# Kernel tuning notes

Measured on AMD Instinct MI355X. Metric: run time of the kernel, lower is better.

## Reference

```python
import jax, jax.numpy as jnp
import numpy as np

B, S, E, DK, DV = 8, 2048, 1024, 512, 512
MASK = True


def setup_inputs() -> dict:
    key = jax.random.key(0)
    ks = jax.random.split(key, 12)
    def xavier(k, shape):
        fan_in, fan_out = shape[1], shape[0]
        lim = float(np.sqrt(6.0 / (fan_in + fan_out)))
        return jax.random.uniform(k, shape, jnp.float32, -lim, lim)
    return {
        "x": jax.random.normal(ks[0], (B, S, E), jnp.float32),
        "Wq_w": xavier(ks[1], (DK, E)),
        "Wq_b": jax.random.normal(ks[2], (DK,), jnp.float32) * 0.02,
        "Wk_w": xavier(ks[3], (DK, E)),
        "Wk_b": jax.random.normal(ks[4], (DK,), jnp.float32) * 0.02,
        "Wv_w": xavier(ks[5], (DV, E)),
        "Wv_b": jax.random.normal(ks[6], (DV,), jnp.float32) * 0.02,
        "alphaq": jax.random.normal(ks[7], (S,), jnp.float32) * 0.1,
        "alphav": jax.random.normal(ks[8], (S,), jnp.float32) * 0.1,
        "tokenq": xavier(ks[9], (DK, DK)),
        "tokenv": xavier(ks[10], (DV, DV)),
    }


def reference(x, Wq_w, Wq_b, Wk_w, Wk_b, Wv_w, Wv_b, alphaq, alphav, tokenq, tokenv):
    dk = Wk_w.shape[0]
    seq_len = x.shape[1]
    Q = jnp.einsum("bse,ke->bsk", x, Wq_w) + Wq_b
    K = jnp.einsum("bse,ke->bsk", x, Wk_w) + Wk_b
    V = jnp.einsum("bse,ve->bsv", x, Wv_w) + Wv_b

    # token-aware temperatures: tanh(tokenX @ gelu(X)^T)^T == tanh(gelu(X) @ tokenX^T)
    token_temp_q = jnp.tanh(jnp.einsum("bsj,ij->bsi", jax.nn.gelu(Q, approximate=False), tokenq))
    token_temp_v = jnp.tanh(jnp.einsum("bsj,ij->bsi", jax.nn.gelu(V, approximate=False), tokenv))

    # argmax/gather knobs: [B,S,S] scores -> K_max per query
    attn_map_exps = jnp.einsum("bqk,bsk->bqs", Q, K)
    max_ids = jnp.argmax(attn_map_exps, axis=2)                    # [B,S]
    K_max = jnp.take_along_axis(K, max_ids[:, :, None], axis=1)    # [B,S,DK]
    K_sum = jnp.sum(K, axis=1, keepdims=True)                      # [B,1,DK]
    knobs = jnp.abs(Q * (K_sum - seq_len * K_max))                 # [B,S,DK]

    log_pos = jnp.log(jnp.arange(1, seq_len + 1, dtype=jnp.float32))[None, :, None]  # [1,S,1]
    position_temp_q = 1.0 + jax.nn.sigmoid(alphaq[None, :, None] - knobs) * log_pos
    position_temp_v = 1.0 + jax.nn.sigmoid(alphav)[None, :, None] * log_pos

    gated_Q = (position_temp_q + token_temp_q) * Q
    gated_V = (position_temp_v + token_temp_v) * V

    attention_wts = jnp.einsum("bqk,bsk->bqs", gated_Q, K) / jnp.sqrt(jnp.float32(dk))
    if MASK:
        causal = jnp.triu(jnp.ones((seq_len, seq_len), dtype=bool), k=1)
        attention_wts = jnp.where(causal[None], -jnp.inf, attention_wts)
    attention_scores = jax.nn.softmax(attention_wts.astype(jnp.float32), axis=-1)
    return jnp.einsum("bqs,bsv->bqv", attention_scores, gated_V)
```

## Files before the change

kernel.cpp:

```cpp
#include <hip/hip_runtime.h>
#include <hip/hip_bf16.h>
#include <math.h>

typedef unsigned short u16;
typedef __attribute__((ext_vector_type(8))) short bhalf8;
typedef __attribute__((ext_vector_type(4))) float floatx4;

#define MFMA16(a,b,c) __builtin_amdgcn_mfma_f32_16x16x32_bf16((a),(b),(c),0,0,0)

__device__ __forceinline__ float bf2f(u16 u){ return __uint_as_float(((unsigned)u)<<16); }
__device__ __forceinline__ u16 f2bf(float f){
  unsigned u = __float_as_uint(f);
  u += 0x7fffu + ((u>>16)&1u);
  return (u16)(u>>16);
}
__device__ __forceinline__ float gelu_f(float x){ return 0.5f*x*(1.0f+erff(x*0.70710678118654752f)); }
__device__ __forceinline__ float sigm(float x){ return 1.0f/(1.0f+__expf(-x)); }

__global__ __launch_bounds__(256) void init_counts(int* cnt){
  if (threadIdx.x == 0 && blockIdx.x == 0) *cnt = 0;
}

__global__ __launch_bounds__(256) void cvt_f32_bf16(const float* __restrict__ src,
                                                    u16* __restrict__ dst, int n){
  int i = (blockIdx.x*256 + threadIdx.x)*4;
  if (i >= n) return;
  const float4 v = *(const float4*)(src + i);
  ushort4 o;
  o.x = f2bf(v.x); o.y = f2bf(v.y); o.z = f2bf(v.z); o.w = f2bf(v.w);
  *(ushort4*)(dst + i) = o;
}

__global__ __launch_bounds__(256) void cvt_split(const float* __restrict__ src,
                                                 u16* __restrict__ dsth,
                                                 u16* __restrict__ dstl, int n){
  int i = (blockIdx.x*256 + threadIdx.x)*4;
  if (i >= n) return;
  const float4 v = *(const float4*)(src + i);
  float vv[4] = {v.x, v.y, v.z, v.w};
  ushort4 oh, ol;
  u16 h;
  h = f2bf(vv[0]); oh.x = h; ol.x = f2bf(vv[0] - bf2f(h));
  h = f2bf(vv[1]); oh.y = h; ol.y = f2bf(vv[1] - bf2f(h));
  h = f2bf(vv[2]); oh.z = h; ol.z = f2bf(vv[2] - bf2f(h));
  h = f2bf(vv[3]); oh.w = h; ol.w = f2bf(vv[3] - bf2f(h));
  *(ushort4*)(dsth + i) = oh;
  *(ushort4*)(dstl + i) = ol;
}

template<int SPLIT>
__global__ __launch_bounds__(256) void gemm_qkvT(
    const u16* __restrict__ xh, const u16* __restrict__ xl,
    const u16* __restrict__ Whh, const u16* __restrict__ Whl,
    const float* __restrict__ bq, const float* __restrict__ bk, const float* __restrict__ bv,
    float* __restrict__ Qf, float* __restrict__ Kf, u16* __restrict__ Vb)
{
  __shared__ __align__(16) u16 Ah[128][72];
  __shared__ __align__(16) u16 Bh[128][72];
  __shared__ __align__(16) u16 Al[SPLIT?128:1][72];
  __shared__ __align__(16) u16 Bl[SPLIT?128:1][72];
  const int tid = threadIdx.x;
  const int lane = tid & 63, wid = tid >> 6;
  const int l15 = lane & 15, lg = lane >> 4;
  const int wr = wid >> 1, wc = wid & 1;
  const int m0 = blockIdx.y * 128;
  const int n0 = blockIdx.x * 128 + (SPLIT ? 0 : 1024);
  const int which = n0 >> 9;
  const int nb = n0 & 511;
  const float* bias = (which==0) ? bq : (which==1) ? bk : bv;

  floatx4 acc[4][4] = {};

  bhalf8 RAh[4], RBh[4], RAl[4], RBl[4];
  auto loadT = [&](int k0){
    #pragma unroll
    for (int it = 0; it < 4; ++it){
      int e = (tid + it*256)*8;
      int r = e >> 6, c = e & 63;
      size_t ao = (size_t)(m0+r)*1024 + k0 + c;
      size_t bo = (size_t)(n0+r)*1024 + k0 + c;
      RAh[it] = *(const bhalf8*)(xh + ao);
      RBh[it] = *(const bhalf8*)(Whh + bo);
      if (SPLIT){
        RAl[it] = *(const bhalf8*)(xl + ao);
        RBl[it] = *(const bhalf8*)(Whl + bo);
      }
    }
  };
  auto writeT = [&](){
    #pragma unroll
    for (int it = 0; it < 4; ++it){
      int e = (tid + it*256)*8;
      int r = e >> 6, c = e & 63;
      *(bhalf8*)&Ah[r][c] = RAh[it];
      *(bhalf8*)&Bh[r][c] = RBh[it];
      if (SPLIT){
        *(bhalf8*)&Al[r][c] = RAl[it];
        *(bhalf8*)&Bl[r][c] = RBl[it];
      }
    }
  };

  loadT(0);
  writeT();
  __syncthreads();
  for (int k0 = 0; k0 < 1024; k0 += 64){
    if (k0 < 960) loadT(k0 + 64);
    #pragma unroll
    for (int kk = 0; kk < 2; ++kk){
      bhalf8 ah[4], bh8[4];
      #pragma unroll
      for (int xx=0; xx<4; xx++){
        ah[xx]  = *(const bhalf8*)&Ah[wr*64 + xx*16 + l15][kk*32 + lg*8];
        bh8[xx] = *(const bhalf8*)&Bh[wc*64 + xx*16 + l15][kk*32 + lg*8];
      }
      if (SPLIT){
        bhalf8 al[4], bl8[4];
        #pragma unroll
        for (int xx=0; xx<4; xx++){
          al[xx]  = *(const bhalf8*)&Al[wr*64 + xx*16 + l15][kk*32 + lg*8];
          bl8[xx] = *(const bhalf8*)&Bl[wc*64 + xx*16 + l15][kk*32 + lg*8];
        }
        #pragma unroll
        for (int mi=0;mi<4;mi++)
          #pragma unroll
          for (int ni=0;ni<4;ni++){
            acc[mi][ni] = MFMA16(ah[mi], bh8[ni], acc[mi][ni]);
            acc[mi][ni] = MFMA16(ah[mi], bl8[ni], acc[mi][ni]);
            acc[mi][ni] = MFMA16(al[mi], bh8[ni], acc[mi][ni]);
          }
      } else {
        #pragma unroll
        for (int mi=0;mi<4;mi++)
          #pragma unroll
          for (int ni=0;ni<4;ni++)
            acc[mi][ni] = MFMA16(ah[mi], bh8[ni], acc[mi][ni]);
      }
    }
    __syncthreads();
    if (k0 < 960){
      writeT();
      __syncthreads();
    }
  }

  #pragma unroll
  for (int mi=0;mi<4;mi++)
    #pragma unroll
    for (int ni=0;ni<4;ni++){
      int cc = nb + wc*64 + ni*16 + l15;
      float bias_v = bias[cc];
      #pragma unroll
      for (int i=0;i<4;i++){
        int row = m0 + wr*64 + mi*16 + lg*4 + i;
        float v = acc[mi][ni][i] + bias_v;
        size_t off = (size_t)row*512 + cc;
        if (which==0){ Qf[off] = v; }
        else if (which==1){ Kf[off] = v; }
        else { Vb[off] = f2bf(v); }
      }
    }
}

__global__ __launch_bounds__(256) void gemm_tanh2(
    const float* __restrict__ Af, const u16* __restrict__ Ab,
    const u16* __restrict__ Bq, const u16* __restrict__ Bv,
    u16* __restrict__ oq, u16* __restrict__ ov)
{
  __shared__ __align__(16) u16 As[128][72];
  __shared__ __align__(16) u16 Bs[128][72];
  const int tid = threadIdx.x;
  const int lane = tid & 63, wid = tid >> 6;
  const int l15 = lane & 15, lg = lane >> 4;
  const int wr = wid >> 1, wc = wid & 1;
  const int m0 = blockIdx.y * 128, n0 = blockIdx.x * 128;
  const int zp = blockIdx.z;
  const u16* B = zp ? Bv : Bq;
  u16* o0 = zp ? ov : oq;

  floatx4 acc[4][4] = {};

  float4 RAf[8]; bhalf8 RAb[4]; bhalf8 RB[4];
  auto loadT = [&](int k0){
    #pragma unroll
    for (int it=0; it<4; ++it){
      int e = (tid + it*256)*8;
      int r = e >> 6, c = e & 63;
      if (zp == 0){
        const float* src = Af + (size_t)(m0+r)*512 + k0 + c;
        RAf[it*2]   = *(const float4*)src;
        RAf[it*2+1] = *(const float4*)(src+4);
      } else {
        RAb[it] = *(const bhalf8*)(Ab + (size_t)(m0+r)*512 + k0 + c);
      }
      RB[it] = *(const bhalf8*)(B + (size_t)(n0+r)*512 + k0 + c);
    }
  };
  auto writeT = [&](){
    #pragma unroll
    for (int it=0; it<4; ++it){
      int e = (tid + it*256)*8;
      int r = e >> 6, c = e & 63;
      bhalf8 g;
      if (zp == 0){
        float vv[8] = {RAf[it*2].x,RAf[it*2].y,RAf[it*2].z,RAf[it*2].w,
                       RAf[it*2+1].x,RAf[it*2+1].y,RAf[it*2+1].z,RAf[it*2+1].w};
        #pragma unroll
        for (int j=0;j<8;j++) g[j] = (short)f2bf(gelu_f(vv[j]));
      } else {
        #pragma unroll
        for (int j=0;j<8;j++) g[j] = (short)f2bf(gelu_f(bf2f((u16)RAb[it][j])));
      }
      *(bhalf8*)&As[r][c] = g;
      *(bhalf8*)&Bs[r][c] = RB[it];
    }
  };

  loadT(0);
  writeT();
  __syncthreads();
  for (int k0 = 0; k0 < 512; k0 += 64){
    if (k0 < 448) loadT(k0 + 64);
    #pragma unroll
    for (int kk = 0; kk < 2; ++kk){
      bhalf8 af[4], bfr[4];
      #pragma unroll
      for (int xx=0;xx<4;xx++) af[xx]  = *(const bhalf8*)&As[wr*64 + xx*16 + l15][kk*32 + lg*8];
      #pragma unroll
      for (int xx=0;xx<4;xx++) bfr[xx] = *(const bhalf8*)&Bs[wc*64 + xx*16 + l15][kk*32 + lg*8];
      #pragma unroll
      for (int mi=0;mi<4;mi++)
        #pragma unroll
        for (int ni=0;ni<4;ni++)
          acc[mi][ni] = MFMA16(af[mi], bfr[ni], acc[mi][ni]);
    }
    __syncthreads();
    if (k0 < 448){
      writeT();
      __syncthreads();
    }
  }

  #pragma unroll
  for (int mi=0;mi<4;mi++)
    #pragma unroll
    for (int ni=0;ni<4;ni++){
      int coln = n0 + wc*64 + ni*16 + l15;
      #pragma unroll
      for (int i=0;i<4;i++){
        int row = m0 + wr*64 + mi*16 + lg*4 + i;
        o0[(size_t)row*512 + coln] = f2bf(tanhf(acc[mi][ni][i]));
      }
    }
}

__global__ __launch_bounds__(256) void gemm_argmax(
    const u16* __restrict__ Qsh, const u16* __restrict__ Qsl,
    const u16* __restrict__ Ksh, const u16* __restrict__ Ksl,
    float4* __restrict__ part)
{
  __shared__ __align__(16) u16 Ah[128][40];
  __shared__ __align__(16) u16 Al[128][40];
  __shared__ __align__(16) u16 Bh[128][40];
  __shared__ __align__(16) u16 Bl[128][40];
  const int tid = threadIdx.x;
  const int lane = tid & 63, wid = tid >> 6;
  const int l15 = lane & 15, lg = lane >> 4;
  const int wr = wid >> 1, wc = wid & 1;
  const int lin = blockIdx.x + 16*blockIdx.y + 256*blockIdx.z;
  const int swz = (lin & 7)*256 + (lin >> 3);
  const int zb  = swz >> 8;
  const int rem = swz & 255;
  const int m0 = (rem >> 4) * 128;
  const int n0 = (rem & 15) * 128;
  const size_t bo = (size_t)zb * 2048 * 512;

  floatx4 acc[4][4] = {};

  bhalf8 RQh[2], RQl[2], RKh[2], RKl[2];
  auto loadT = [&](int k0){
    #pragma unroll
    for (int it = 0; it < 2; ++it){
      int e = (tid + it*256)*8;
      int r = e >> 5, c = e & 31;
      size_t qo = bo + (size_t)(m0+r)*512 + k0 + c;
      size_t ko = bo + (size_t)(n0+r)*512 + k0 + c;
      RQh[it] = *(const bhalf8*)(Qsh + qo);
      RQl[it] = *(const bhalf8*)(Qsl + qo);
      RKh[it] = *(const bhalf8*)(Ksh + ko);
      RKl[it] = *(const bhalf8*)(Ksl + ko);
    }
  };
  auto writeT = [&](){
    #pragma unroll
    for (int it = 0; it < 2; ++it){
      int e = (tid + it*256)*8;
      int r = e >> 5, c = e & 31;
      *(bhalf8*)&Ah[r][c] = RQh[it];
      *(bhalf8*)&Al[r][c] = RQl[it];
      *(bhalf8*)&Bh[r][c] = RKh[it];
      *(bhalf8*)&Bl[r][c] = RKl[it];
    }
  };

  loadT(0);
  writeT();
  __syncthreads();
  for (int k0 = 0; k0 < 512; k0 += 32){
    if (k0 < 480) loadT(k0 + 32);
    {
      bhalf8 ah[4], al[4], bh[4], bl[4];
      #pragma unroll
      for (int xx=0;xx<4;xx++){
        ah[xx] = *(const bhalf8*)&Ah[wr*64 + xx*16 + l15][lg*8];
        al[xx] = *(const bhalf8*)&Al[wr*64 + xx*16 + l15][lg*8];
        bh[xx] = *(const bhalf8*)&Bh[wc*64 + xx*16 + l15][lg*8];
        bl[xx] = *(const bhalf8*)&Bl[wc*64 + xx*16 + l15][lg*8];
      }
      #pragma unroll
      for (int mi=0;mi<4;mi++)
        #pragma unroll
        for (int ni=0;ni<4;ni++){
          acc[mi][ni] = MFMA16(ah[mi], bh[ni], acc[mi][ni]);
          acc[mi][ni] = MFMA16(ah[mi], bl[ni], acc[mi][ni]);
          acc[mi][ni] = MFMA16(al[mi], bh[ni], acc[mi][ni]);
        }
    }
    __syncthreads();
    if (k0 < 480){
      writeT();
      __syncthreads();
    }
  }

  #pragma unroll
  for (int mi=0;mi<4;mi++)
    #pragma unroll
    for (int i=0;i<4;i++){
      float v1 = -INFINITY, v2 = -INFINITY; int i1 = 0x7fffffff;
      #pragma unroll
      for (int ni=0;ni<4;ni++){
        float v = acc[mi][ni][i];
        int col = n0 + wc*64 + ni*16 + l15;
        if (v > v1 || (v == v1 && col < i1)){ v2 = v1; v1 = v; i1 = col; }
        else v2 = fmaxf(v2, v);
      }
      #pragma unroll
      for (int ms=1; ms<16; ms<<=1){
        float w1 = __shfl_xor(v1, ms, 64);
        int   j1 = __shfl_xor(i1, ms, 64);
        float w2 = __shfl_xor(v2, ms, 64);
        if (w1 > v1 || (w1 == v1 && j1 < i1)){ v2 = fmaxf(v1, w2); v1 = w1; i1 = j1; }
        else { v2 = fmaxf(v2, w1); }
      }
      if (l15 == 0){
        int row = m0 + wr*64 + mi*16 + lg*4 + i;
        size_t gm = (size_t)zb*2048 + row;
        part[gm*32 + ((n0>>7)<<1) + wc] = make_float4(v1, __int_as_float(i1), v2, 0.0f);
      }
    }
}

__global__ __launch_bounds__(256) void argmax_reduce(const float4* __restrict__ part,
                                                     int* __restrict__ ids,
                                                     int* __restrict__ list1,
                                                     int* __restrict__ cnt){
  int r = blockIdx.x*256 + threadIdx.x;
  if (r >= 16384) return;
  float v1 = -INFINITY, v2 = -INFINITY; int i1 = 0x7fffffff;
  #pragma unroll
  for (int t=0;t<32;t++){
    float4 p = part[(size_t)r*32 + t];
    float w1 = p.x, w2 = p.z; int j1 = __float_as_int(p.y);
    if (w1 > v1 || (w1 == v1 && j1 < i1)){ v2 = fmaxf(v1, w2); v1 = w1; i1 = j1; }
    else { v2 = fmaxf(v2, w1); }
  }
  ids[r] = i1;
  if (v1 - v2 < 0.02f){
    int k = atomicAdd(cnt, 1);
    if (k < 16384) list1[k] = r;
  }
}

__global__ __launch_bounds__(256) void argmax_fix(
    const float* __restrict__ Qf, const float* __restrict__ Kf,
    const int* __restrict__ list1, const int* __restrict__ cnt,
    int* __restrict__ ids)
{
  __shared__ float q[512];
  __shared__ double rbest[256];
  __shared__ int ridx[256];
  const int tid = threadIdx.x;
  const int n = *cnt;
  for (int j = blockIdx.x; j < n; j += gridDim.x){
    const int r = list1[j];
    const int b = r >> 11;
    __syncthreads();
    for (int d = tid; d < 512; d += 256) q[d] = Qf[(size_t)r*512 + d];
    __syncthreads();
    double best = -1e300; int bi = 0x7fffffff;
    for (int c = 0; c < 8; ++c){
      int key = tid + c*256;
      const float* kr = Kf + ((size_t)b*2048 + key)*512;
      double acc = 0.0;
      for (int e = 0; e < 512; ++e) acc += (double)q[e]*(double)kr[e];
      if (acc > best || (acc == best && key < bi)){ best = acc; bi = key; }
    }
    rbest[tid] = best; ridx[tid] = bi;
    __syncthreads();
    for (int st=128; st>0; st>>=1){
      if (tid < st){
        double ov = rbest[tid+st]; int oi = ridx[tid+st];
        if (ov > rbest[tid] || (ov == rbest[tid] && oi < ridx[tid])){ rbest[tid]=ov; ridx[tid]=oi; }
      }
      __syncthreads();
    }
    if (tid == 0) ids[r] = ridx[0];
    __syncthreads();
  }
}

__global__ __launch_bounds__(256) void ksum_part(const float* __restrict__ Kf,
                                                 float* __restrict__ kpart){
  const int b = blockIdx.x, chunk = blockIdx.y;
  const int tid = threadIdx.x;
  const float* base = Kf + (size_t)b*2048*512 + (size_t)chunk*128*512;
  #pragma unroll
  for (int h = 0; h < 2; ++h){
    int col = tid + h*256;
    double s = 0.0;
    for (int r = 0; r < 128; ++r) s += (double)base[(size_t)r*512 + col];
    kpart[((size_t)b*16 + chunk)*512 + col] = (float)s;
  }
}
__global__ __launch_bounds__(256) void ksum_final(const float* __restrict__ kpart,
                                                  float* __restrict__ Ksum){
  const int b = blockIdx.x >> 1;
  const int col = (blockIdx.x & 1)*256 + threadIdx.x;
  double s = 0.0;
  #pragma unroll
  for (int c = 0; c < 16; ++c) s += (double)kpart[((size_t)b*16 + c)*512 + col];
  Ksum[b*512 + col] = (float)s;
}

__global__ __launch_bounds__(256) void gating_kernel(
    const float* Qf, const float* __restrict__ Kf,
    const u16* __restrict__ V,
    const u16* __restrict__ ttq, const u16* __restrict__ ttv,
    const int* __restrict__ ids, const float* __restrict__ Ksum,
    const float* __restrict__ alphaq, const float* __restrict__ alphav,
    u16* __restrict__ gQh, u16* __restrict__ gQl, float* gVf)
{
  const int m = blockIdx.x;
  const int b = m >> 11, s = m & 2047;
  const int mid = ids[m];
  const float lp = __logf((float)(s+1));
  const float aq = alphaq[s];
  const float pv = 1.0f + sigm(alphav[s])*lp;
  const float qscale = 0.044194173824159220f;
  const size_t ro = (size_t)m*512;
  const size_t ko = ((size_t)b*2048 + mid)*512;
  const int k0 = threadIdx.x*2;

  float2 ks2 = *(const float2*)(Ksum + b*512 + k0);
  float2 q2  = *(const float2*)(Qf + ro + k0);
  float2 km2 = *(const float2*)(Kf + ko + k0);
  ushort2 v2 = *(const ushort2*)(V + ro + k0);
  ushort2 tq2 = *(const ushort2*)(ttq + ro + k0);
  ushort2 tv2 = *(const ushort2*)(ttv + ro + k0);
  ushort2 oqh, oql;
  float2 ov;
  {
    float knob = fabsf(q2.x*(ks2.x - 2048.0f*km2.x));
    float ptq = 1.0f + sigm(aq - knob)*lp;
    float oq = (ptq + bf2f(tq2.x))*q2.x*qscale;
    u16 h = f2bf(oq); oqh.x = h; oql.x = f2bf(oq - bf2f(h));
    ov.x = (pv + bf2f(tv2.x))*bf2f(v2.x);
  }
  {
    float knob = fabsf(q2.y*(ks2.y - 2048.0f*km2.y));
    float ptq = 1.0f + sigm(aq - knob)*lp;
    float oq = (ptq + bf2f(tq2.y))*q2.y*qscale;
    u16 h = f2bf(oq); oqh.y = h; oql.y = f2bf(oq - bf2f(h));
    ov.y = (pv + bf2f(tv2.y))*bf2f(v2.y);
  }
  *(ushort2*)(gQh + ro + k0) = oqh;
  *(ushort2*)(gQl + ro + k0) = oql;
  *(float2*)(gVf + ro + k0) = ov;
}

__global__ __launch_bounds__(256) void transpose_v(const float* __restrict__ src,
                                                   u16* __restrict__ dst){
  __shared__ __align__(16) u16 t[64][72];
  const int b = blockIdx.z;
  const int s0 = blockIdx.x*64, v0 = blockIdx.y*64;
  const float* S = src + (size_t)b*2048*512;
  u16* D = dst + (size_t)b*512*2048;
  const int tid = threadIdx.x;
  #pragma unroll
  for (int it=0; it<2; ++it){
    int e = (tid + it*256)*8;
    int r = e>>6, c = e&63;
    const float* p = S + (size_t)(s0+r)*512 + v0 + c;
    float4 u0 = *(const float4*)p;
    float4 u1 = *(const float4*)(p+4);
    float vv[8] = {u0.x,u0.y,u0.z,u0.w,u1.x,u1.y,u1.z,u1.w};
    bhalf8 o;
    #pragma unroll
    for (int j=0;j<8;j++) o[j] = (short)f2bf(vv[j]);
    *(bhalf8*)&t[r][c] = o;
  }
  __syncthreads();
  #pragma unroll
  for (int it=0; it<2; ++it){
    int e = (tid + it*256)*8;
    int r = e>>6, c = e&63;
    bhalf8 o;
    #pragma unroll
    for (int j=0;j<8;j++) o[j] = (short)t[c+j][r];
    *(bhalf8*)(D + (size_t)(v0+r)*2048 + s0 + c) = o;
  }
}

#define QSW(r,g) ((((g) ^ ((r)&7))) << 3)
__global__ __launch_bounds__(256, 2) void flash6(
    const u16* __restrict__ gQh, const u16* __restrict__ gQl,
    const u16* __restrict__ Khb, const u16* __restrict__ Klb,
    const u16* __restrict__ gVT, float* __restrict__ Out)
{
  const int bx = blockIdx.x;
  const int by = blockIdx.y;
  const int b  = by;
  const int hh = (bx & 1) ? (63 - (bx >> 1)) : (bx >> 1);
  const int qt = (by < 4) ? hh : (63 - hh);
  const int q0 = qt * 32;
  const int tid = threadIdx.x, lane = tid & 63, wid = tid >> 6;
  const int l15 = lane & 15, lg = lane >> 4;
  const int wr = wid >> 1, wc = wid & 1;

  __shared__ __align__(16) char smem[74112];
  u16*   qhs = (u16*)smem;
  u16*   khs = (u16*)(smem + 32768);
  u16*   kls = (u16*)(smem + 40960);
  u16*   vss = (u16*)(smem + 49152);
  float* sf  = (float*)(smem + 49152);
  u16*   phs = (u16*)(smem + 65536);
  float* mstat = (float*)(smem + 73728);
  float* lstat = mstat + 32;
  float* osc   = mstat + 64;

  const u16* Qhb = gQh + ((size_t)b*2048 + q0)*512;
  const u16* Khbb = Khb + (size_t)b*2048*512;
  const u16* Klbb = Klb + (size_t)b*2048*512;
  const u16* Vtb = gVT + (size_t)b*512*2048;

  #pragma unroll
  for (int it=0; it<8; ++it){
    int e = (tid + it*256)*8;
    int r = e >> 9, c = e & 511;
    bhalf8 hv = *(const bhalf8*)(Qhb + (size_t)r*512 + c);
    *(bhalf8*)&qhs[r*512 + QSW(r, c>>3)] = hv;
  }
  bhalf8 qlr[16];
  {
    const u16* Qlb = gQl + ((size_t)b*2048 + q0 + wr*16 + l15)*512;
    #pragma unroll
    for (int c=0;c<8;c++)
      #pragma unroll
      for (int kk=0;kk<2;kk++)
        qlr[c*2+kk] = *(const bhalf8*)(Qlb + c*64 + kk*32 + lg*8);
  }
  if (tid < 32){ mstat[tid] = -INFINITY; lstat[tid] = 0.0f; }

  floatx4 O[4][2][2] = {};
  __syncthreads();

  auto loadK = [&](int kt, int c, bhalf8* dh, bhalf8* dl){
    #pragma unroll
    for (int it=0; it<2; ++it){
      int e = (tid + it*256)*8;
      int r = e>>6, cc = e&63;
      size_t off = (size_t)(kt*64+r)*512 + c*64 + cc;
      dh[it] = *(const bhalf8*)(Khbb + off);
      dl[it] = *(const bhalf8*)(Klbb + off);
    }
  };
  auto writeK = [&](const bhalf8* sh, const bhalf8* sl){
    #pragma unroll
    for (int it=0; it<2; ++it){
      int e = (tid + it*256)*8;
      int r = e>>6, cc = e&63;
      int o = r*64 + QSW(r, cc>>3);
      *(bhalf8*)&khs[o] = sh[it];
      *(bhalf8*)&kls[o] = sl[it];
    }
  };
  auto loadV = [&](int kt, int vc, bhalf8* dst){
    #pragma unroll
    for (int it=0; it<4; ++it){
      int e = (tid + it*256)*8;
      int r = e>>6, cc = e&63;
      dst[it] = *(const bhalf8*)(Vtb + (size_t)(vc*128+r)*2048 + kt*64 + cc);
    }
  };
  auto writeV = [&](const bhalf8* src){
    #pragma unroll
    for (int it=0; it<4; ++it){
      int e = (tid + it*256)*8;
      int r = e>>6, cc = e&63;
      *(bhalf8*)&vss[r*64 + QSW(r, cc>>3)] = src[it];
    }
  };

  const int qrow = wr*16 + l15;
  const int srow = tid >> 3, seg = tid & 7;

  const int nkt = (q0 + 31)/64 + 1;
  for (int kt = 0; kt < nkt; ++kt){
    floatx4 sacc[2] = {};
    bhalf8 kha[2], kla[2];
    loadK(kt, 0, kha, kla);
    writeK(kha, kla);
    __syncthreads();
    for (int c = 0; c < 8; ++c){
      bhalf8 khb2[2], klb2[2];
      if (c < 7) loadK(kt, c+1, khb2, klb2);
      #pragma unroll
      for (int kk=0; kk<2; ++kk){
        bhalf8 ah = *(const bhalf8*)&qhs[qrow*512 + QSW(qrow, c*8 + kk*4 + lg)];
        bhalf8 al = qlr[c*2+kk];
        #pragma unroll
        for (int ni=0; ni<2; ++ni){
          int krow = wc*32 + ni*16 + l15;
          int o = krow*64 + QSW(krow, kk*4 + lg);
          bhalf8 bh = *(const bhalf8*)&khs[o];
          bhalf8 bl = *(const bhalf8*)&kls[o];
          sacc[ni] = MFMA16(ah, bh, sacc[ni]);
          sacc[ni] = MFMA16(ah, bl, sacc[ni]);
          sacc[ni] = MFMA16(al, bh, sacc[ni]);
        }
      }
      __syncthreads();
      if (c < 7){
        writeK(khb2, klb2);
        __syncthreads();
      }
    }
    #pragma unroll
    for (int ni=0; ni<2; ++ni)
      #pragma unroll
      for (int i=0;i<4;i++){
        int row = wr*16 + lg*4 + i;
        int col = wc*32 + ni*16 + l15;
        sf[row*66 + col] = (kt*64 + col <= q0 + row) ? sacc[ni][i] : -INFINITY;
      }
    __syncthreads();
    bhalf8 va[4];
    loadV(kt, 0, va);
    {
      float pv8[8];
      float tmax = -INFINITY;
      #pragma unroll
      for (int jx=0;jx<8;jx++){ pv8[jx] = sf[srow*66 + seg*8 + jx]; tmax = fmaxf(tmax, pv8[jx]); }
      tmax = fmaxf(tmax, __shfl_xor(tmax,1,64));
      tmax = fmaxf(tmax, __shfl_xor(tmax,2,64));
      tmax = fmaxf(tmax, __shfl_xor(tmax,4,64));
      float mo = mstat[srow];
      float mn = fmaxf(mo, tmax);
      float ss = 0.0f;
      bhalf8 h8;
      #pragma unroll
      for (int jx=0;jx<8;jx++){
        float p = __expf(pv8[jx] - mn);
        ss += p;
        h8[jx] = (short)f2bf(p);
      }
      ss += __shfl_xor(ss,1,64);
      ss += __shfl_xor(ss,2,64);
      ss += __shfl_xor(ss,4,64);
      int o = srow*64 + QSW(srow, seg);
      *(bhalf8*)&phs[o] = h8;
      if (seg == 0){
        float sc = __expf(mo - mn);
        lstat[srow] = lstat[srow]*sc + ss;
        mstat[srow] = mn;
        osc[srow] = sc;
      }
    }
    __syncthreads();
    #pragma unroll
    for (int mi=0;mi<2;mi++)
      #pragma unroll
      for (int i=0;i<4;i++){
        float s = osc[mi*16 + lg*4 + i];
        #pragma unroll
        for (int vc=0; vc<4; ++vc)
          #pragma unroll
          for (int ni=0;ni<2;ni++)
            O[vc][mi][ni][i] *= s;
      }
    writeV(va);
    __syncthreads();
    for (int vc = 0; vc < 4; ++vc){
      bhalf8 vb_[4];
      if (vc < 3) loadV(kt, vc+1, vb_);
      #pragma unroll
      for (int kk=0; kk<2; ++kk){
        int gp = kk*4 + lg;
        bhalf8 pah0 = *(const bhalf8*)&phs[l15*64 + QSW(l15, gp)];
        bhalf8 pah1 = *(const bhalf8*)&phs[(16+l15)*64 + QSW(16+l15, gp)];
        #pragma unroll
        for (int ni=0; ni<2; ++ni){
          int vrow = wid*32 + ni*16 + l15;
          bhalf8 bv_ = *(const bhalf8*)&vss[vrow*64 + QSW(vrow, gp)];
          O[vc][0][ni] = MFMA16(pah0, bv_, O[vc][0][ni]);
          O[vc][1][ni] = MFMA16(pah1, bv_, O[vc][1][ni]);
        }
      }
      __syncthreads();
      if (vc < 3){
        writeV(vb_);
        __syncthreads();
      }
    }
  }

  #pragma unroll
  for (int vc=0; vc<4; ++vc)
    #pragma unroll
    for (int mi=0;mi<2;mi++)
      #pragma unroll
      for (int i=0;i<4;i++){
        int r = mi*16 + lg*4 + i;
        float inv = 1.0f / lstat[r];
        #pragma unroll
        for (int ni=0;ni<2;ni++){
          int v = vc*128 + wid*32 + ni*16 + l15;
          Out[((size_t)b*2048 + q0 + r)*512 + v] = O[vc][mi][ni][i] * inv;
        }
      }
}

extern "C" void kernel_launch(void* const* d_in, const int* in_sizes, int n_in,
                              void* d_out, int out_size, void* d_ws, size_t ws_size,
                              hipStream_t stream)
{
  const float* x   = (const float*)d_in[0];
  const float* Wq  = (const float*)d_in[1];
  const float* bq  = (const float*)d_in[2];
  const float* Wk  = (const float*)d_in[3];
  const float* bk  = (const float*)d_in[4];
  const float* Wv  = (const float*)d_in[5];
  const float* bv  = (const float*)d_in[6];
  const float* alphaq = (const float*)d_in[7];
  const float* alphav = (const float*)d_in[8];
  const float* tokq = (const float*)d_in[9];
  const float* tokv = (const float*)d_in[10];
  float* out = (float*)d_out;
  char* ws = (char*)d_ws;

  float* Qf  = (float*)(ws + 0);
  float* gVf = Qf;
  u16* Khb   = (u16*)(ws + 0);
  u16* Klb   = (u16*)(ws + 16777216);
  float* Kf  = (float*)(ws + 33554432);
  u16* Vb    = (u16*)(ws + 67108864);
  u16* ttq   = (u16*)(ws + 83886080);
  u16* gVT   = ttq;
  u16* Ksh   = (u16*)(ws + 83886080);
  u16* ttv   = (u16*)(ws + 100663296);
  u16* Ksl   = (u16*)(ws + 100663296);
  u16* xl    = (u16*)(ws + 83886080);
  u16* gQh   = (u16*)(ws + 117440512);
  u16* Qsh   = (u16*)(ws + 117440512);
  u16* gQl   = (u16*)(ws + 134217728);
  u16* Qsl   = (u16*)(ws + 134217728);
  u16* xh    = (u16*)(ws + 117440512);
  u16* tq_b  = (u16*)(ws + 150994944);
  u16* tv_b  = (u16*)(ws + 151519232);
  int* ids   = (int*)(ws + 152043520);
  float* ksum = (float*)(ws + 152109056);
  float4* part = (float4*)(ws + 152125440);
  u16* Whh   = (u16*)(ws + 152125440);
  u16* Whl   = (u16*)(ws + 155271168);
  int* list1 = (int*)(ws + 160514048);
  int* cnt   = (int*)(ws + 160579584);
  float* kpart = (float*)(ws + 160579840);
  (void)ws_size; (void)in_sizes; (void)n_in; (void)out_size;

  init_counts<<<1,256,0,stream>>>(cnt);
  cvt_f32_bf16<<<256,256,0,stream>>>(tokq, tq_b, 262144);
  cvt_f32_bf16<<<256,256,0,stream>>>(tokv, tv_b, 262144);

  cvt_split<<<16384,256,0,stream>>>(x,  xh, xl, 16777216);
  cvt_split<<<512,256,0,stream>>>(Wq, Whh,            Whl,            524288);
  cvt_split<<<512,256,0,stream>>>(Wk, Whh + 524288,   Whl + 524288,   524288);
  cvt_split<<<512,256,0,stream>>>(Wv, Whh + 1048576,  Whl + 1048576,  524288);

  gemm_qkvT<1><<<dim3(8,128),256,0,stream>>>(xh, xl, Whh, Whl, bq, bk, bv, Qf, Kf, Vb);
  gemm_qkvT<0><<<dim3(4,128),256,0,stream>>>(xh, xl, Whh, Whl, bq, bk, bv, Qf, Kf, Vb);

  cvt_split<<<8192,256,0,stream>>>(Qf, Qsh, Qsl, 8388608);
  cvt_split<<<8192,256,0,stream>>>(Kf, Ksh, Ksl, 8388608);

  gemm_argmax<<<dim3(16,16,8),256,0,stream>>>(Qsh, Qsl, Ksh, Ksl, part);

  gemm_tanh2<<<dim3(4,128,2),256,0,stream>>>(Qf, Vb, tq_b, tv_b, ttq, ttv);

  argmax_reduce<<<64,256,0,stream>>>(part, ids, list1, cnt);
  argmax_fix<<<64,256,0,stream>>>(Qf, Kf, list1, cnt, ids);

  ksum_part<<<dim3(8,16),256,0,stream>>>(Kf, kpart);
  ksum_final<<<16,256,0,stream>>>(kpart, ksum);

  gating_kernel<<<16384,256,0,stream>>>(Qf, Kf, Vb, ttq, ttv, ids, ksum,
                                        alphaq, alphav, gQh, gQl, gVf);

  transpose_v<<<dim3(32,8,8),256,0,stream>>>(gVf, gVT);

  cvt_split<<<8192,256,0,stream>>>(Kf, Khb, Klb, 8388608);

  flash6<<<dim3(64,8),256,0,stream>>>(gQh, gQl, Khb, Klb, gVT, out);
}
```

Measured before the change: 932.9 us.

## Drop K low-part split in flash kernel and double-buffer K tiles

The flash attention kernel now uses only the bf16 high part of K, removing the Q_hi*K_lo MFMA term and the K low-half loads and LDS storage. K tiles are double-buffered in shared memory, with the next chunk prefetched into registers, so one barrier per chunk is removed. The K conversion becomes a single bf16 cast instead of a hi/lo split. This lowers memory traffic and MFMA work but reduces the precision of the attention scores.

```diff
diff --git a/kernel.cpp b/kernel.cpp
--- a/kernel.cpp
+++ b/kernel.cpp
@@ -523,9 +523,9 @@
 }
 
 #define QSW(r,g) ((((g) ^ ((r)&7))) << 3)
-__global__ __launch_bounds__(256, 2) void flash6(
+__global__ __launch_bounds__(256, 2) void flash7(
     const u16* __restrict__ gQh, const u16* __restrict__ gQl,
-    const u16* __restrict__ Khb, const u16* __restrict__ Klb,
+    const u16* __restrict__ Khb,
     const u16* __restrict__ gVT, float* __restrict__ Out)
 {
   const int bx = blockIdx.x;
@@ -538,20 +538,17 @@
   const int l15 = lane & 15, lg = lane >> 4;
   const int wr = wid >> 1, wc = wid & 1;
 
-  __shared__ __align__(16) char smem[74112];
+  __shared__ __align__(16) char smem[69888];
   u16*   qhs = (u16*)smem;
-  u16*   khs = (u16*)(smem + 32768);
-  u16*   kls = (u16*)(smem + 40960);
+  float* sf  = (float*)(smem + 32768);
   u16*   vss = (u16*)(smem + 49152);
-  float* sf  = (float*)(smem + 49152);
   u16*   phs = (u16*)(smem + 65536);
-  float* mstat = (float*)(smem + 73728);
+  float* mstat = (float*)(smem + 69632);
   float* lstat = mstat + 32;
   float* osc   = mstat + 64;
 
   const u16* Qhb = gQh + ((size_t)b*2048 + q0)*512;
-  const u16* Khbb = Khb + (size_t)b*2048*512;
-  const u16* Klbb = Klb + (size_t)b*2048*512;
+  const u16* Kbb = Khb + (size_t)b*2048*512;
   const u16* Vtb = gVT + (size_t)b*512*2048;
 
   #pragma unroll
@@ -575,24 +572,22 @@
   floatx4 O[4][2][2] = {};
   __syncthreads();
 
-  auto loadK = [&](int kt, int c, bhalf8* dh, bhalf8* dl){
+  bhalf8 RK[2];
+  auto loadK = [&](int kt, int c){
     #pragma unroll
     for (int it=0; it<2; ++it){
       int e = (tid + it*256)*8;
       int r = e>>6, cc = e&63;
-      size_t off = (size_t)(kt*64+r)*512 + c*64 + cc;
-      dh[it] = *(const bhalf8*)(Khbb + off);
-      dl[it] = *(const bhalf8*)(Klbb + off);
-    }
-  };
-  auto writeK = [&](const bhalf8* sh, const bhalf8* sl){
+      RK[it] = *(const bhalf8*)(Kbb + (size_t)(kt*64+r)*512 + c*64 + cc);
+    }
+  };
+  auto writeK = [&](int buf){
+    u16* khX = (u16*)(smem + 32768 + buf*8192);
     #pragma unroll
     for (int it=0; it<2; ++it){
       int e = (tid + it*256)*8;
       int r = e>>6, cc = e&63;
-      int o = r*64 + QSW(r, cc>>3);
-      *(bhalf8*)&khs[o] = sh[it];
-      *(bhalf8*)&kls[o] = sl[it];
+      *(bhalf8*)&khX[r*64 + QSW(r, cc>>3)] = RK[it];
     }
   };
   auto loadV = [&](int kt, int vc, bhalf8* dst){
@@ -618,13 +613,12 @@
   const int nkt = (q0 + 31)/64 + 1;
   for (int kt = 0; kt < nkt; ++kt){
     floatx4 sacc[2] = {};
-    bhalf8 kha[2], kla[2];
-    loadK(kt, 0, kha, kla);
-    writeK(kha, kla);
-    __syncthreads();
+    loadK(kt, 0); writeK(0); loadK(kt, 1);
+    __syncthreads();
+    #pragma unroll
     for (int c = 0; c < 8; ++c){
-      bhalf8 khb2[2], klb2[2];
-      if (c < 7) loadK(kt, c+1, khb2, klb2);
+      const int cur = c & 1;
+      u16* khX = (u16*)(smem + 32768 + cur*8192);
       #pragma unroll
       for (int kk=0; kk<2; ++kk){
         bhalf8 ah = *(const bhalf8*)&qhs[qrow*512 + QSW(qrow, c*8 + kk*4 + lg)];
@@ -632,19 +626,16 @@
         #pragma unroll
         for (int ni=0; ni<2; ++ni){
           int krow = wc*32 + ni*16 + l15;
-          int o = krow*64 + QSW(krow, kk*4 + lg);
-          bhalf8 bh = *(const bhalf8*)&khs[o];
-          bhalf8 bl = *(const bhalf8*)&kls[o];
+          bhalf8 bh = *(const bhalf8*)&khX[krow*64 + QSW(krow, kk*4 + lg)];
           sacc[ni] = MFMA16(ah, bh, sacc[ni]);
-          sacc[ni] = MFMA16(ah, bl, sacc[ni]);
           sacc[ni] = MFMA16(al, bh, sacc[ni]);
         }
       }
+      if (c < 7){
+        writeK(cur ^ 1);
+        if (c < 6) loadK(kt, c+2);
+      }
       __syncthreads();
-      if (c < 7){
-        writeK(khb2, klb2);
-        __syncthreads();
-      }
     }
     #pragma unroll
     for (int ni=0; ni<2; ++ni)
@@ -762,7 +753,6 @@
   float* Qf  = (float*)(ws + 0);
   float* gVf = Qf;
   u16* Khb   = (u16*)(ws + 0);
-  u16* Klb   = (u16*)(ws + 16777216);
   float* Kf  = (float*)(ws + 33554432);
   u16* Vb    = (u16*)(ws + 67108864);
   u16* ttq   = (u16*)(ws + 83886080);
@@ -818,7 +808,7 @@
 
   transpose_v<<<dim3(32,8,8),256,0,stream>>>(gVf, gVT);
 
-  cvt_split<<<8192,256,0,stream>>>(Kf, Khb, Klb, 8388608);
-
-  flash6<<<dim3(64,8),256,0,stream>>>(gQh, gQl, Khb, Klb, gVT, out);
-}
+  cvt_f32_bf16<<<8192,256,0,stream>>>(Kf, Khb, 8388608);
+
+  flash7<<<dim3(64,8),256,0,stream>>>(gQh, gQl, Khb, gVT, out);
+}
```

Measured after the change: 855.2 us. 1.09x faster.
